# Kernel optimization log

Hardware: AMD Instinct MI355X
Metric: run time of the kernel (lower is better)

Reference implementation:

```python
import jax, jax.numpy as jnp
import numpy as np

EMBED = 1024
HEADS = 16
HEAD_DIM = EMBED // HEADS


def setup_inputs() -> dict:
    key = jax.random.key(0)
    ks = jax.random.split(key, 7)
    B, S = 4, 2048
    q = jax.random.normal(ks[0], (B, S, EMBED), dtype=jnp.float32)
    k = jax.random.normal(ks[1], (B, S, EMBED), dtype=jnp.float32)
    v = jax.random.normal(ks[2], (B, S, EMBED), dtype=jnp.float32)
    # causal mask, broadcast over heads: [B, 1, S, S]
    mask = jnp.broadcast_to(jnp.tril(jnp.ones((S, S), dtype=jnp.int32))[None, None], (B, 1, S, S))
    scale = 1.0 / np.sqrt(EMBED)
    w_q = jax.random.normal(ks[3], (EMBED, EMBED), dtype=jnp.float32) * scale
    w_k = jax.random.normal(ks[4], (EMBED, EMBED), dtype=jnp.float32) * scale
    w_v = jax.random.normal(ks[5], (EMBED, EMBED), dtype=jnp.float32) * scale
    w_o = jax.random.normal(ks[6], (EMBED, EMBED), dtype=jnp.float32) * scale
    return {"q": q, "k": k, "v": v, "mask": mask,
            "w_q": w_q, "w_k": w_k, "w_v": w_v, "w_o": w_o}


def reference(q, k, v, mask, w_q, w_k, w_v, w_o):
    B, S, _ = q.shape
    # Linear projections (torch Linear: x @ W^T), split into heads: [B,H,S,D]
    def proj(x, w):
        return (x @ w.T).reshape(B, -1, HEADS, HEAD_DIM).transpose(0, 2, 1, 3)
    qh, kh, vh = proj(q, w_q), proj(k, w_k), proj(v, w_v)
    scores = jnp.einsum('bhqd,bhkd->bhqk', qh, kh) / jnp.sqrt(jnp.float32(HEAD_DIM))
    scores = jnp.where(mask == 0, jnp.float32(-1e9), scores)
    attn = jax.nn.softmax(scores, axis=-1)
    # dropout is identity in eval/reference mode
    x = jnp.einsum('bhqk,bhkd->bhqd', attn, vh)  # [B,H,S,D]
    x = x.transpose(0, 2, 1, 3).reshape(B, S, HEADS * HEAD_DIM)
    return x @ w_o.T
```

## Files before the change

kernel.cpp:

```cpp
#include <hip/hip_runtime.h>

typedef unsigned short u16;
typedef __attribute__((ext_vector_type(8))) short v8s;
typedef __attribute__((ext_vector_type(4))) float v4f;

#define S_LEN  2048
#define NHEADS 16
#define DHEAD  64
#define EMB    1024

#if __has_builtin(__builtin_amdgcn_exp2f)
#define EXP2F __builtin_amdgcn_exp2f
#else
#define EXP2F exp2f
#endif

__device__ __forceinline__ u16 f32_bf16(float f) {
  union { float f; unsigned u; } x; x.f = f;
  unsigned r = x.u + 0x7fffu + ((x.u >> 16) & 1u);
  return (u16)(r >> 16);
}

__device__ __forceinline__ void async16(const void* g, void* l) {
  __builtin_amdgcn_global_load_lds(
      (const __attribute__((address_space(1))) unsigned int*)g,
      (__attribute__((address_space(3))) unsigned int*)l, 16, 0, 0);
}

__global__ __launch_bounds__(256) void cvt_all(
    const float4* __restrict__ s0, const float4* __restrict__ s1,
    const float4* __restrict__ s2, const float4* __restrict__ s3,
    const float4* __restrict__ s4, const float4* __restrict__ s5,
    const float4* __restrict__ s6,
    u16* __restrict__ d0, u16* __restrict__ d1,
    u16* __restrict__ d2, u16* __restrict__ d3,
    u16* __restrict__ d4, u16* __restrict__ d5,
    u16* __restrict__ d6, int nbig, int nsmall) {
  const int y = blockIdx.y;
  const float4* s; u16* d;
  switch (y) {
    case 0: s = s0; d = d0; break;  case 1: s = s1; d = d1; break;
    case 2: s = s2; d = d2; break;  case 3: s = s3; d = d3; break;
    case 4: s = s4; d = d4; break;  case 5: s = s5; d = d5; break;
    default: s = s6; d = d6; break;
  }
  const int n8 = (y < 3) ? nbig : nsmall;
  for (int i = blockIdx.x * 256 + threadIdx.x; i < n8; i += gridDim.x * 256) {
    const float4 lo = s[2 * i];
    const float4 hi = s[2 * i + 1];
    v8s o;
    o[0] = (short)f32_bf16(lo.x); o[1] = (short)f32_bf16(lo.y);
    o[2] = (short)f32_bf16(lo.z); o[3] = (short)f32_bf16(lo.w);
    o[4] = (short)f32_bf16(hi.x); o[5] = (short)f32_bf16(hi.y);
    o[6] = (short)f32_bf16(hi.z); o[7] = (short)f32_bf16(hi.w);
    *(v8s*)(d + (size_t)i * 8) = o;
  }
}

template <int MODE>
__global__ __launch_bounds__(1024, 4) void gemm2ph(
    const u16* __restrict__ A, const u16* __restrict__ W0,
    const u16* __restrict__ W1, const u16* __restrict__ W2,
    u16* __restrict__ Cq, u16* __restrict__ Ck, u16* __restrict__ Cv,
    float* __restrict__ Cf, int mtiles) {
  const int K = 1024;
  const int NKT = 16;
  __shared__ __align__(16) u16 lA[2][256 * 64];
  __shared__ __align__(16) u16 lB[2][128 * 64];
  const int t = threadIdx.x;
  const int lane = t & 63, wv = t >> 6;
  const int wm = wv >> 2, wn = wv & 3;
  const int qr = lane >> 4, cl = lane & 15;

  const int nwg = gridDim.x;
  const int sid = (blockIdx.x & 7) * (nwg >> 3) + (blockIdx.x >> 3);
  const int bm = sid % mtiles, bn = sid / mtiles;
  const int m0 = bm << 8, n0 = bn << 7;
  const int sec = (MODE == 0) ? (m0 >> 13) : 0;
  const u16* W =
      (MODE == 0) ? ((sec == 0) ? W0 : (sec == 1) ? W1 : W2) : W0;

  v4f acc[4][2];
#pragma unroll
  for (int i = 0; i < 4; ++i)
#pragma unroll
    for (int j = 0; j < 2; ++j) acc[i][j] = (v4f){0.f, 0.f, 0.f, 0.f};

  const int srow = t >> 3;
  const int swe = ((t & 7) ^ (srow & 7)) << 3;
  const u16* aS0 = A + (size_t)(m0 + srow) * K + swe;
  const u16* aS1 = A + (size_t)(m0 + 128 + srow) * K + swe;
  const u16* bS  = W + (size_t)(n0 + srow) * K + swe;

  async16(aS0, &lA[0][t << 3]);
  async16(aS1, &lA[0][(t + 1024) << 3]);
  async16(bS,  &lB[0][t << 3]);
  __syncthreads();

  for (int kt = 0; kt < NKT; ++kt) {
    const int cur = kt & 1;
    if (kt + 1 < NKT) {
      const int off = (kt + 1) << 6;
      async16(aS0 + off, &lA[1 - cur][t << 3]);
      async16(aS1 + off, &lA[1 - cur][(t + 1024) << 3]);
      async16(bS + off,  &lB[1 - cur][t << 3]);
    }
    v8s a[4][2], b[2][2];
#pragma unroll
    for (int mf = 0; mf < 4; ++mf)
#pragma unroll
      for (int kh = 0; kh < 2; ++kh) {
        const int R = wm * 64 + mf * 16 + cl;
        a[mf][kh] =
            *(const v8s*)&lA[cur][R * 64 + ((((kh << 2) + qr) ^ (R & 7)) << 3)];
      }
#pragma unroll
    for (int nf = 0; nf < 2; ++nf)
#pragma unroll
      for (int kh = 0; kh < 2; ++kh) {
        const int R = wn * 32 + nf * 16 + cl;
        b[nf][kh] =
            *(const v8s*)&lB[cur][R * 64 + ((((kh << 2) + qr) ^ (R & 7)) << 3)];
      }
    __builtin_amdgcn_s_setprio(1);
#pragma unroll
    for (int kh = 0; kh < 2; ++kh)
#pragma unroll
      for (int mf = 0; mf < 4; ++mf)
#pragma unroll
        for (int nf = 0; nf < 2; ++nf)
          acc[mf][nf] = __builtin_amdgcn_mfma_f32_16x16x32_bf16(
              a[mf][kh], b[nf][kh], acc[mf][nf], 0, 0, 0);
    __builtin_amdgcn_s_setprio(0);
    __syncthreads();
  }

  if constexpr (MODE == 0) {
    u16* C = (sec == 0) ? Cq : (sec == 1) ? Ck : Cv;
#pragma unroll
    for (int mf = 0; mf < 4; ++mf)
#pragma unroll
      for (int nf = 0; nf < 2; ++nf)
#pragma unroll
        for (int r = 0; r < 4; ++r) {
          const int mloc = (m0 & 8191) + wm * 64 + mf * 16 + qr * 4 + r;
          const int n = n0 + wn * 32 + nf * 16 + cl;
          const int bb = mloc >> 11, s = mloc & (S_LEN - 1);
          const int h = n >> 6, d = n & (DHEAD - 1);
          const size_t idx =
              (sec < 2) ? (((size_t)bb * NHEADS + h) * S_LEN + s) * DHEAD + d
                        : (((size_t)bb * NHEADS + h) * DHEAD + d) * S_LEN + s;
          C[idx] = f32_bf16(acc[mf][nf][r]);
        }
  } else {
#pragma unroll
    for (int mf = 0; mf < 4; ++mf)
#pragma unroll
      for (int nf = 0; nf < 2; ++nf)
#pragma unroll
        for (int r = 0; r < 4; ++r) {
          const int m = m0 + wm * 64 + mf * 16 + qr * 4 + r;
          const int n = n0 + wn * 32 + nf * 16 + cl;
          Cf[(size_t)m * 1024 + n] = acc[mf][nf][r];
        }
  }
}

__global__ __launch_bounds__(256, 2) void attn_causal(
    const u16* __restrict__ Qp, const u16* __restrict__ Kp,
    const u16* __restrict__ VpT, u16* __restrict__ Out) {
  __shared__ __align__(16) u16 lK[2][2][64 * 64];
  __shared__ __align__(16) u16 lV[2][2][64 * 64];
  __shared__ __align__(16) u16 pb[4][32 * 64];
  const int t = threadIdx.x;
  const int lane = t & 63, w = t >> 6;
  const int qr = lane >> 4, cl = lane & 15;
  const int id = blockIdx.x;
  const int col = (id & 7) + ((id >> 6) << 3);
  const int pair = (id >> 3) & 7;
  const int h = col & 15, b = col >> 4;
  const size_t bh = ((size_t)b * NHEADS + h) * S_LEN * DHEAD;
  const u16* Qb = Qp + bh;
  const u16* Kb = Kp + bh;
  const u16* Vb = VpT + bh;

  v8s vone;
#pragma unroll
  for (int j = 0; j < 8; ++j) vone[j] = (short)0x3F80;
  const float SC = 0.125f * 1.4426950408889634f;

#define STAGE_T(TILE, GP, SL)                                                 \
  do {                                                                        \
    const int kn_ = (TILE) << 6;                                              \
    _Pragma("unroll") for (int i_ = 0; i_ < 2; ++i_) {                        \
      const int c_ = t + (i_ << 8);                                           \
      const int krow_ = c_ >> 3, kdc_ = (c_ & 7) ^ (krow_ & 7);               \
      async16(Kb + (size_t)(kn_ + krow_) * DHEAD + kdc_ * 8,                  \
              &lK[GP][SL][(w * 64 + (i_ << 8)) * 8]);                         \
      const int vd_ = c_ >> 3, vkc_ = (c_ & 7) ^ (vd_ & 7);                   \
      async16(Vb + (size_t)vd_ * S_LEN + kn_ + vkc_ * 8,                      \
              &lV[GP][SL][(w * 64 + (i_ << 8)) * 8]);                         \
    }                                                                         \
  } while (0)

  for (int phase = 0; phase < 2; ++phase) {
    const int qt = phase == 0 ? (15 - pair) : pair;
    const int q0 = qt << 7;
    const int wr0 = q0 + w * 32;

    v8s aq[2][2];
#pragma unroll
    for (int mf = 0; mf < 2; ++mf)
#pragma unroll
      for (int kf = 0; kf < 2; ++kf)
        aq[mf][kf] = *(const v8s*)(Qb + (size_t)(wr0 + mf * 16 + cl) * DHEAD +
                                   kf * 32 + qr * 8);

    v4f o[2][4], lac[2];
#pragma unroll
    for (int mf = 0; mf < 2; ++mf) {
      lac[mf] = (v4f){0.f, 0.f, 0.f, 0.f};
#pragma unroll
      for (int nf = 0; nf < 4; ++nf) o[mf][nf] = (v4f){0.f, 0.f, 0.f, 0.f};
    }

    const int ngrp = qt + 1;
    __syncthreads();
    STAGE_T(0, 0, 0);
    STAGE_T(1, 0, 1);

    for (int g = 0; g < ngrp; ++g) {
      const int gp = g & 1;
      __syncthreads();
      if (g + 1 < ngrp) {
        STAGE_T(2 * g + 2, 1 - gp, 0);
        STAGE_T(2 * g + 3, 1 - gp, 1);
      }
#pragma unroll
      for (int sl = 0; sl < 2; ++sl) {
        const int kt = 2 * g + sl;
        const int k0 = kt << 6;
        if (k0 > wr0 + 31) continue;
        const u16* lKc = &lK[gp][sl][0];
        const u16* lVc = &lV[gp][sl][0];

        v4f sacc[2][4];
#pragma unroll
        for (int mf = 0; mf < 2; ++mf)
#pragma unroll
          for (int ni = 0; ni < 4; ++ni) sacc[mf][ni] = (v4f){0.f, 0.f, 0.f, 0.f};
#pragma unroll
        for (int kf = 0; kf < 2; ++kf)
#pragma unroll
          for (int ni = 0; ni < 4; ++ni) {
            const v8s bk = *(const v8s*)&lKc[((ni * 16 + cl) * 8 +
                                             (((kf << 2) + qr) ^ (cl & 7))) * 8];
            sacc[0][ni] = __builtin_amdgcn_mfma_f32_16x16x32_bf16(
                aq[0][kf], bk, sacc[0][ni], 0, 0, 0);
            sacc[1][ni] = __builtin_amdgcn_mfma_f32_16x16x32_bf16(
                aq[1][kf], bk, sacc[1][ni], 0, 0, 0);
          }

#pragma unroll
        for (int mf = 0; mf < 2; ++mf) {
          const int rowb0 = wr0 + mf * 16;
          if (k0 + 63 <= rowb0) {
#pragma unroll
            for (int ni = 0; ni < 4; ++ni) {
              const int kc = ni * 2 + (cl >> 3);
#pragma unroll
              for (int r = 0; r < 4; ++r) {
                const float e = EXP2F(sacc[mf][ni][r] * SC);
                pb[w][((kc * 32 + mf * 16 + r * 4 + qr) << 3) + (cl & 7)] =
                    (u16)(__float_as_uint(e) >> 16);
              }
            }
          } else {
            const int rowb = rowb0 + qr * 4;
#pragma unroll
            for (int ni = 0; ni < 4; ++ni) {
              const int colk = k0 + ni * 16 + cl;
              const int kc = ni * 2 + (cl >> 3);
#pragma unroll
              for (int r = 0; r < 4; ++r) {
                float e = EXP2F(sacc[mf][ni][r] * SC);
                if (colk > rowb + r) e = 0.f;
                pb[w][((kc * 32 + mf * 16 + r * 4 + qr) << 3) + (cl & 7)] =
                    (u16)(__float_as_uint(e) >> 16);
              }
            }
          }
        }

#pragma unroll
        for (int kf = 0; kf < 2; ++kf) {
          const int kc = (kf << 2) + qr;
          const int sig0 = ((cl & 3) << 2) + (cl >> 2);
          const v8s ap0 = *(const v8s*)&pb[w][((kc * 32 + sig0) << 3)];
          const v8s ap1 = *(const v8s*)&pb[w][((kc * 32 + 16 + sig0) << 3)];
          lac[0] = __builtin_amdgcn_mfma_f32_16x16x32_bf16(ap0, vone, lac[0], 0, 0, 0);
          lac[1] = __builtin_amdgcn_mfma_f32_16x16x32_bf16(ap1, vone, lac[1], 0, 0, 0);
#pragma unroll
          for (int nf = 0; nf < 4; ++nf) {
            const v8s bv = *(const v8s*)&lVc[((nf * 16 + cl) * 8 +
                                             (kc ^ (cl & 7))) * 8];
            o[0][nf] = __builtin_amdgcn_mfma_f32_16x16x32_bf16(ap0, bv, o[0][nf], 0, 0, 0);
            o[1][nf] = __builtin_amdgcn_mfma_f32_16x16x32_bf16(ap1, bv, o[1][nf], 0, 0, 0);
          }
        }
      }
    }

#pragma unroll
    for (int mf = 0; mf < 2; ++mf) {
      float inv[4];
#pragma unroll
      for (int r = 0; r < 4; ++r) inv[r] = 1.0f / lac[mf][r];
#pragma unroll
      for (int nf = 0; nf < 4; ++nf)
#pragma unroll
        for (int r = 0; r < 4; ++r) {
          const int row = wr0 + mf * 16 + qr * 4 + r;
          const int colo = h * DHEAD + nf * 16 + cl;
          Out[((size_t)b * S_LEN + row) * EMB + colo] = f32_bf16(o[mf][nf][r] * inv[r]);
        }
    }
  }
#undef STAGE_T
}

extern "C" void kernel_launch(void* const* d_in, const int* in_sizes, int n_in,
                              void* d_out, int out_size, void* d_ws, size_t ws_size,
                              hipStream_t stream) {
  (void)in_sizes; (void)n_in; (void)out_size; (void)ws_size;
  const float* q  = (const float*)d_in[0];
  const float* k  = (const float*)d_in[1];
  const float* v  = (const float*)d_in[2];
  const float* wq = (const float*)d_in[4];
  const float* wk = (const float*)d_in[5];
  const float* wv = (const float*)d_in[6];
  const float* wo = (const float*)d_in[7];
  float* out = (float*)d_out;

  const size_t MT = (size_t)4 * S_LEN * EMB;
  const size_t WT = (size_t)EMB * EMB;
  u16* p = (u16*)d_ws;
  u16* xq = p; p += MT;
  u16* xk = p; p += MT;
  u16* xv = p; p += MT;
  u16* wqb = p; p += WT;
  u16* wkb = p; p += WT;
  u16* wvb = p; p += WT;
  u16* wob = p; p += WT;
  u16* Qp = p; p += MT;
  u16* Kp = p; p += MT;
  u16* Vp = p; p += MT;
  u16* Ao = xq;

  hipLaunchKernelGGL(cvt_all, dim3(512, 7), dim3(256), 0, stream,
                     (const float4*)q, (const float4*)k, (const float4*)v,
                     (const float4*)wq, (const float4*)wk, (const float4*)wv,
                     (const float4*)wo,
                     xq, xk, xv, wqb, wkb, wvb, wob,
                     (int)(MT / 8), (int)(WT / 8));
  hipLaunchKernelGGL((gemm2ph<0>), dim3(768), dim3(1024), 0, stream,
                     xq, wqb, wkb, wvb, Qp, Kp, Vp, (float*)nullptr, 96);
  hipLaunchKernelGGL(attn_causal, dim3(512), dim3(256), 0, stream,
                     Qp, Kp, Vp, Ao);
  hipLaunchKernelGGL((gemm2ph<1>), dim3(256), dim3(1024), 0, stream,
                     Ao, wob, (const u16*)nullptr, (const u16*)nullptr,
                     (u16*)nullptr, (u16*)nullptr, (u16*)nullptr, out, 32);
}
```

Measured before the change: 352.3 us.

## Shrink GEMM tiles to 128x128 and use 8 waves of 16 rows in attention

The projection GEMMs move from 256x128 tiles with 1024 threads to 128x128 tiles with 512 threads, doubling the grid and halving LDS per block. The attention kernel goes from 4 waves of 32 query rows each to 8 waves of 16 rows each, so per-wave accumulators and P buffers shrink and one K/V staging load per thread covers the tile. The goal is more parallelism and better occupancy, at the cost of less data reuse per K/V tile load and more global traffic in the GEMMs.

```diff
diff --git a/kernel.cpp b/kernel.cpp
--- a/kernel.cpp
+++ b/kernel.cpp
@@ -58,14 +58,14 @@
 }
 
 template <int MODE>
-__global__ __launch_bounds__(1024, 4) void gemm2ph(
+__global__ __launch_bounds__(512, 2) void gemm2ph(
     const u16* __restrict__ A, const u16* __restrict__ W0,
     const u16* __restrict__ W1, const u16* __restrict__ W2,
     u16* __restrict__ Cq, u16* __restrict__ Ck, u16* __restrict__ Cv,
     float* __restrict__ Cf, int mtiles) {
   const int K = 1024;
   const int NKT = 16;
-  __shared__ __align__(16) u16 lA[2][256 * 64];
+  __shared__ __align__(16) u16 lA[2][128 * 64];
   __shared__ __align__(16) u16 lB[2][128 * 64];
   const int t = threadIdx.x;
   const int lane = t & 63, wv = t >> 6;
@@ -75,7 +75,7 @@
   const int nwg = gridDim.x;
   const int sid = (blockIdx.x & 7) * (nwg >> 3) + (blockIdx.x >> 3);
   const int bm = sid % mtiles, bn = sid / mtiles;
-  const int m0 = bm << 8, n0 = bn << 7;
+  const int m0 = bm << 7, n0 = bn << 7;
   const int sec = (MODE == 0) ? (m0 >> 13) : 0;
   const u16* W =
       (MODE == 0) ? ((sec == 0) ? W0 : (sec == 1) ? W1 : W2) : W0;
@@ -87,23 +87,31 @@
     for (int j = 0; j < 2; ++j) acc[i][j] = (v4f){0.f, 0.f, 0.f, 0.f};
 
   const int srow = t >> 3;
-  const int swe = ((t & 7) ^ (srow & 7)) << 3;
-  const u16* aS0 = A + (size_t)(m0 + srow) * K + swe;
-  const u16* aS1 = A + (size_t)(m0 + 128 + srow) * K + swe;
-  const u16* bS  = W + (size_t)(n0 + srow) * K + swe;
-
-  async16(aS0, &lA[0][t << 3]);
-  async16(aS1, &lA[0][(t + 1024) << 3]);
-  async16(bS,  &lB[0][t << 3]);
+  const int sw = ((t & 7) ^ (srow & 7)) << 3;
+  const u16* aS[2];
+  const u16* bS[2];
+#pragma unroll
+  for (int u = 0; u < 2; ++u) {
+    aS[u] = A + (size_t)(m0 + srow + u * 64) * K + sw;
+    bS[u] = W + (size_t)(n0 + srow + u * 64) * K + sw;
+  }
+
+#pragma unroll
+  for (int u = 0; u < 2; ++u) async16(aS[u], &lA[0][(t + (u << 9)) << 3]);
+#pragma unroll
+  for (int u = 0; u < 2; ++u) async16(bS[u], &lB[0][(t + (u << 9)) << 3]);
   __syncthreads();
 
   for (int kt = 0; kt < NKT; ++kt) {
     const int cur = kt & 1;
     if (kt + 1 < NKT) {
       const int off = (kt + 1) << 6;
-      async16(aS0 + off, &lA[1 - cur][t << 3]);
-      async16(aS1 + off, &lA[1 - cur][(t + 1024) << 3]);
-      async16(bS + off,  &lB[1 - cur][t << 3]);
+#pragma unroll
+      for (int u = 0; u < 2; ++u)
+        async16(aS[u] + off, &lA[1 - cur][(t + (u << 9)) << 3]);
+#pragma unroll
+      for (int u = 0; u < 2; ++u)
+        async16(bS[u] + off, &lB[1 - cur][(t + (u << 9)) << 3]);
     }
     v8s a[4][2], b[2][2];
 #pragma unroll
@@ -166,12 +174,12 @@
   }
 }
 
-__global__ __launch_bounds__(256, 2) void attn_causal(
+__global__ __launch_bounds__(512, 2) void attn_causal(
     const u16* __restrict__ Qp, const u16* __restrict__ Kp,
     const u16* __restrict__ VpT, u16* __restrict__ Out) {
   __shared__ __align__(16) u16 lK[2][2][64 * 64];
   __shared__ __align__(16) u16 lV[2][2][64 * 64];
-  __shared__ __align__(16) u16 pb[4][32 * 64];
+  __shared__ __align__(16) u16 pb[8][16 * 64];
   const int t = threadIdx.x;
   const int lane = t & 63, w = t >> 6;
   const int qr = lane >> 4, cl = lane & 15;
@@ -192,37 +200,25 @@
 #define STAGE_T(TILE, GP, SL)                                                 \
   do {                                                                        \
     const int kn_ = (TILE) << 6;                                              \
-    _Pragma("unroll") for (int i_ = 0; i_ < 2; ++i_) {                        \
-      const int c_ = t + (i_ << 8);                                           \
-      const int krow_ = c_ >> 3, kdc_ = (c_ & 7) ^ (krow_ & 7);               \
-      async16(Kb + (size_t)(kn_ + krow_) * DHEAD + kdc_ * 8,                  \
-              &lK[GP][SL][(w * 64 + (i_ << 8)) * 8]);                         \
-      const int vd_ = c_ >> 3, vkc_ = (c_ & 7) ^ (vd_ & 7);                   \
-      async16(Vb + (size_t)vd_ * S_LEN + kn_ + vkc_ * 8,                      \
-              &lV[GP][SL][(w * 64 + (i_ << 8)) * 8]);                         \
-    }                                                                         \
+    const int r_ = t >> 3, c_ = (t & 7) ^ (r_ & 7);                           \
+    async16(Kb + (size_t)(kn_ + r_) * DHEAD + c_ * 8, &lK[GP][SL][t * 8]);    \
+    async16(Vb + (size_t)r_ * S_LEN + kn_ + c_ * 8, &lV[GP][SL][t * 8]);      \
   } while (0)
 
   for (int phase = 0; phase < 2; ++phase) {
     const int qt = phase == 0 ? (15 - pair) : pair;
     const int q0 = qt << 7;
-    const int wr0 = q0 + w * 32;
-
-    v8s aq[2][2];
-#pragma unroll
-    for (int mf = 0; mf < 2; ++mf)
-#pragma unroll
-      for (int kf = 0; kf < 2; ++kf)
-        aq[mf][kf] = *(const v8s*)(Qb + (size_t)(wr0 + mf * 16 + cl) * DHEAD +
-                                   kf * 32 + qr * 8);
-
-    v4f o[2][4], lac[2];
-#pragma unroll
-    for (int mf = 0; mf < 2; ++mf) {
-      lac[mf] = (v4f){0.f, 0.f, 0.f, 0.f};
-#pragma unroll
-      for (int nf = 0; nf < 4; ++nf) o[mf][nf] = (v4f){0.f, 0.f, 0.f, 0.f};
-    }
+    const int wr0 = q0 + w * 16;
+
+    v8s aq[2];
+#pragma unroll
+    for (int kf = 0; kf < 2; ++kf)
+      aq[kf] = *(const v8s*)(Qb + (size_t)(wr0 + cl) * DHEAD + kf * 32 + qr * 8);
+
+    v4f o[4], lac;
+    lac = (v4f){0.f, 0.f, 0.f, 0.f};
+#pragma unroll
+    for (int nf = 0; nf < 4; ++nf) o[nf] = (v4f){0.f, 0.f, 0.f, 0.f};
 
     const int ngrp = qt + 1;
     __syncthreads();
@@ -240,54 +236,46 @@
       for (int sl = 0; sl < 2; ++sl) {
         const int kt = 2 * g + sl;
         const int k0 = kt << 6;
-        if (k0 > wr0 + 31) continue;
+        if (k0 > wr0 + 15) continue;
         const u16* lKc = &lK[gp][sl][0];
         const u16* lVc = &lV[gp][sl][0];
 
-        v4f sacc[2][4];
-#pragma unroll
-        for (int mf = 0; mf < 2; ++mf)
-#pragma unroll
-          for (int ni = 0; ni < 4; ++ni) sacc[mf][ni] = (v4f){0.f, 0.f, 0.f, 0.f};
+        v4f sacc[4];
+#pragma unroll
+        for (int ni = 0; ni < 4; ++ni) sacc[ni] = (v4f){0.f, 0.f, 0.f, 0.f};
 #pragma unroll
         for (int kf = 0; kf < 2; ++kf)
 #pragma unroll
           for (int ni = 0; ni < 4; ++ni) {
             const v8s bk = *(const v8s*)&lKc[((ni * 16 + cl) * 8 +
                                              (((kf << 2) + qr) ^ (cl & 7))) * 8];
-            sacc[0][ni] = __builtin_amdgcn_mfma_f32_16x16x32_bf16(
-                aq[0][kf], bk, sacc[0][ni], 0, 0, 0);
-            sacc[1][ni] = __builtin_amdgcn_mfma_f32_16x16x32_bf16(
-                aq[1][kf], bk, sacc[1][ni], 0, 0, 0);
+            sacc[ni] = __builtin_amdgcn_mfma_f32_16x16x32_bf16(
+                aq[kf], bk, sacc[ni], 0, 0, 0);
           }
 
-#pragma unroll
-        for (int mf = 0; mf < 2; ++mf) {
-          const int rowb0 = wr0 + mf * 16;
-          if (k0 + 63 <= rowb0) {
-#pragma unroll
-            for (int ni = 0; ni < 4; ++ni) {
-              const int kc = ni * 2 + (cl >> 3);
-#pragma unroll
-              for (int r = 0; r < 4; ++r) {
-                const float e = EXP2F(sacc[mf][ni][r] * SC);
-                pb[w][((kc * 32 + mf * 16 + r * 4 + qr) << 3) + (cl & 7)] =
-                    (u16)(__float_as_uint(e) >> 16);
-              }
+        if (k0 + 63 <= wr0) {
+#pragma unroll
+          for (int ni = 0; ni < 4; ++ni) {
+            const int kc = ni * 2 + (cl >> 3);
+#pragma unroll
+            for (int r = 0; r < 4; ++r) {
+              const float e = EXP2F(sacc[ni][r] * SC);
+              pb[w][((kc * 16 + r * 4 + qr) << 3) + (cl & 7)] =
+                  (u16)(__float_as_uint(e) >> 16);
             }
-          } else {
-            const int rowb = rowb0 + qr * 4;
-#pragma unroll
-            for (int ni = 0; ni < 4; ++ni) {
-              const int colk = k0 + ni * 16 + cl;
-              const int kc = ni * 2 + (cl >> 3);
-#pragma unroll
-              for (int r = 0; r < 4; ++r) {
-                float e = EXP2F(sacc[mf][ni][r] * SC);
-                if (colk > rowb + r) e = 0.f;
-                pb[w][((kc * 32 + mf * 16 + r * 4 + qr) << 3) + (cl & 7)] =
-                    (u16)(__float_as_uint(e) >> 16);
-              }
+          }
+        } else {
+          const int rowb = wr0 + qr * 4;
+#pragma unroll
+          for (int ni = 0; ni < 4; ++ni) {
+            const int colk = k0 + ni * 16 + cl;
+            const int kc = ni * 2 + (cl >> 3);
+#pragma unroll
+            for (int r = 0; r < 4; ++r) {
+              float e = EXP2F(sacc[ni][r] * SC);
+              if (colk > rowb + r) e = 0.f;
+              pb[w][((kc * 16 + r * 4 + qr) << 3) + (cl & 7)] =
+                  (u16)(__float_as_uint(e) >> 16);
             }
           }
         }
@@ -296,35 +284,29 @@
         for (int kf = 0; kf < 2; ++kf) {
           const int kc = (kf << 2) + qr;
           const int sig0 = ((cl & 3) << 2) + (cl >> 2);
-          const v8s ap0 = *(const v8s*)&pb[w][((kc * 32 + sig0) << 3)];
-          const v8s ap1 = *(const v8s*)&pb[w][((kc * 32 + 16 + sig0) << 3)];
-          lac[0] = __builtin_amdgcn_mfma_f32_16x16x32_bf16(ap0, vone, lac[0], 0, 0, 0);
-          lac[1] = __builtin_amdgcn_mfma_f32_16x16x32_bf16(ap1, vone, lac[1], 0, 0, 0);
+          const v8s ap = *(const v8s*)&pb[w][((kc * 16 + sig0) << 3)];
+          lac = __builtin_amdgcn_mfma_f32_16x16x32_bf16(ap, vone, lac, 0, 0, 0);
 #pragma unroll
           for (int nf = 0; nf < 4; ++nf) {
             const v8s bv = *(const v8s*)&lVc[((nf * 16 + cl) * 8 +
                                              (kc ^ (cl & 7))) * 8];
-            o[0][nf] = __builtin_amdgcn_mfma_f32_16x16x32_bf16(ap0, bv, o[0][nf], 0, 0, 0);
-            o[1][nf] = __builtin_amdgcn_mfma_f32_16x16x32_bf16(ap1, bv, o[1][nf], 0, 0, 0);
+            o[nf] = __builtin_amdgcn_mfma_f32_16x16x32_bf16(ap, bv, o[nf], 0, 0, 0);
           }
         }
       }
     }
 
-#pragma unroll
-    for (int mf = 0; mf < 2; ++mf) {
-      float inv[4];
-#pragma unroll
-      for (int r = 0; r < 4; ++r) inv[r] = 1.0f / lac[mf][r];
-#pragma unroll
-      for (int nf = 0; nf < 4; ++nf)
-#pragma unroll
-        for (int r = 0; r < 4; ++r) {
-          const int row = wr0 + mf * 16 + qr * 4 + r;
-          const int colo = h * DHEAD + nf * 16 + cl;
-          Out[((size_t)b * S_LEN + row) * EMB + colo] = f32_bf16(o[mf][nf][r] * inv[r]);
-        }
-    }
+    float inv[4];
+#pragma unroll
+    for (int r = 0; r < 4; ++r) inv[r] = 1.0f / lac[r];
+#pragma unroll
+    for (int nf = 0; nf < 4; ++nf)
+#pragma unroll
+      for (int r = 0; r < 4; ++r) {
+        const int row = wr0 + qr * 4 + r;
+        const int colo = h * DHEAD + nf * 16 + cl;
+        Out[((size_t)b * S_LEN + row) * EMB + colo] = f32_bf16(o[nf][r] * inv[r]);
+      }
   }
 #undef STAGE_T
 }
@@ -363,11 +345,11 @@
                      (const float4*)wo,
                      xq, xk, xv, wqb, wkb, wvb, wob,
                      (int)(MT / 8), (int)(WT / 8));
-  hipLaunchKernelGGL((gemm2ph<0>), dim3(768), dim3(1024), 0, stream,
-                     xq, wqb, wkb, wvb, Qp, Kp, Vp, (float*)nullptr, 96);
-  hipLaunchKernelGGL(attn_causal, dim3(512), dim3(256), 0, stream,
+  hipLaunchKernelGGL((gemm2ph<0>), dim3(1536), dim3(512), 0, stream,
+                     xq, wqb, wkb, wvb, Qp, Kp, Vp, (float*)nullptr, 192);
+  hipLaunchKernelGGL(attn_causal, dim3(512), dim3(512), 0, stream,
                      Qp, Kp, Vp, Ao);
-  hipLaunchKernelGGL((gemm2ph<1>), dim3(256), dim3(1024), 0, stream,
+  hipLaunchKernelGGL((gemm2ph<1>), dim3(512), dim3(512), 0, stream,
                      Ao, wob, (const u16*)nullptr, (const u16*)nullptr,
-                     (u16*)nullptr, (u16*)nullptr, (u16*)nullptr, out, 32);
-}
+                     (u16*)nullptr, (u16*)nullptr, (u16*)nullptr, out, 64);
+}
```

Result: no change. 345.7 us (-1.9%).

## Restructure GEMMs to 128x128 tiles with intra-block split-K over 8 waves

Applied to the files above, without the earlier changes.

Replaces the 1024-thread 256x128-tile GEMM with a 512-thread 128x128-tile kernel. The eight waves are split into two K-halves of each 64-wide K step, and each wave computes a 64x64 sub-tile. The two halves' partial accumulators are then reduced through LDS before the epilogue. This doubles the number of workgroups and gives each wave a larger per-wave output tile, aiming for better register reuse and occupancy. The cost is an extra LDS reduction pass and half of the waves going idle during the epilogue.

```diff
diff --git a/kernel.cpp b/kernel.cpp
--- a/kernel.cpp
+++ b/kernel.cpp
@@ -58,93 +58,120 @@
 }
 
 template <int MODE>
-__global__ __launch_bounds__(1024, 4) void gemm2ph(
+__global__ __launch_bounds__(512, 2) void gemmks(
     const u16* __restrict__ A, const u16* __restrict__ W0,
     const u16* __restrict__ W1, const u16* __restrict__ W2,
     u16* __restrict__ Cq, u16* __restrict__ Ck, u16* __restrict__ Cv,
     float* __restrict__ Cf, int mtiles) {
   const int K = 1024;
   const int NKT = 16;
-  __shared__ __align__(16) u16 lA[2][256 * 64];
-  __shared__ __align__(16) u16 lB[2][128 * 64];
+  __shared__ __align__(16) u16 ldsbuf[32768];
+  u16* const lA0 = ldsbuf;
+  u16* const lB0 = ldsbuf + 16384;
   const int t = threadIdx.x;
   const int lane = t & 63, wv = t >> 6;
-  const int wm = wv >> 2, wn = wv & 3;
+  const int kh = wv >> 2;
+  const int sp = wv & 3;
+  const int wm = sp >> 1, wn = sp & 1;
   const int qr = lane >> 4, cl = lane & 15;
 
   const int nwg = gridDim.x;
   const int sid = (blockIdx.x & 7) * (nwg >> 3) + (blockIdx.x >> 3);
   const int bm = sid % mtiles, bn = sid / mtiles;
-  const int m0 = bm << 8, n0 = bn << 7;
+  const int m0 = bm << 7, n0 = bn << 7;
   const int sec = (MODE == 0) ? (m0 >> 13) : 0;
   const u16* W =
       (MODE == 0) ? ((sec == 0) ? W0 : (sec == 1) ? W1 : W2) : W0;
 
-  v4f acc[4][2];
+  v4f acc[4][4];
 #pragma unroll
   for (int i = 0; i < 4; ++i)
 #pragma unroll
-    for (int j = 0; j < 2; ++j) acc[i][j] = (v4f){0.f, 0.f, 0.f, 0.f};
+    for (int j = 0; j < 4; ++j) acc[i][j] = (v4f){0.f, 0.f, 0.f, 0.f};
 
   const int srow = t >> 3;
-  const int swe = ((t & 7) ^ (srow & 7)) << 3;
-  const u16* aS0 = A + (size_t)(m0 + srow) * K + swe;
-  const u16* aS1 = A + (size_t)(m0 + 128 + srow) * K + swe;
-  const u16* bS  = W + (size_t)(n0 + srow) * K + swe;
-
-  async16(aS0, &lA[0][t << 3]);
-  async16(aS1, &lA[0][(t + 1024) << 3]);
-  async16(bS,  &lB[0][t << 3]);
+  const int sw = ((t & 7) ^ (srow & 7)) << 3;
+  const u16* aS[2];
+  const u16* bS[2];
+#pragma unroll
+  for (int u = 0; u < 2; ++u) {
+    aS[u] = A + (size_t)(m0 + srow + u * 64) * K + sw;
+    bS[u] = W + (size_t)(n0 + srow + u * 64) * K + sw;
+  }
+
+  int aOff[4], bOff[4];
+#pragma unroll
+  for (int f = 0; f < 4; ++f) {
+    const int Ra = wm * 64 + f * 16 + cl;
+    aOff[f] = Ra * 64 + ((((kh << 2) + qr) ^ (Ra & 7)) << 3);
+    const int Rb = wn * 64 + f * 16 + cl;
+    bOff[f] = Rb * 64 + ((((kh << 2) + qr) ^ (Rb & 7)) << 3);
+  }
+
+#pragma unroll
+  for (int u = 0; u < 2; ++u) async16(aS[u], lA0 + ((t + (u << 9)) << 3));
+#pragma unroll
+  for (int u = 0; u < 2; ++u) async16(bS[u], lB0 + ((t + (u << 9)) << 3));
   __syncthreads();
 
   for (int kt = 0; kt < NKT; ++kt) {
     const int cur = kt & 1;
     if (kt + 1 < NKT) {
       const int off = (kt + 1) << 6;
-      async16(aS0 + off, &lA[1 - cur][t << 3]);
-      async16(aS1 + off, &lA[1 - cur][(t + 1024) << 3]);
-      async16(bS + off,  &lB[1 - cur][t << 3]);
+      u16* dA = lA0 + (1 - cur) * 8192;
+      u16* dB = lB0 + (1 - cur) * 8192;
+#pragma unroll
+      for (int u = 0; u < 2; ++u) async16(aS[u] + off, dA + ((t + (u << 9)) << 3));
+#pragma unroll
+      for (int u = 0; u < 2; ++u) async16(bS[u] + off, dB + ((t + (u << 9)) << 3));
     }
-    v8s a[4][2], b[2][2];
+    const u16* rA = lA0 + cur * 8192;
+    const u16* rB = lB0 + cur * 8192;
+    v8s a[4], b[4];
+#pragma unroll
+    for (int f = 0; f < 4; ++f) a[f] = *(const v8s*)(rA + aOff[f]);
+#pragma unroll
+    for (int f = 0; f < 4; ++f) b[f] = *(const v8s*)(rB + bOff[f]);
+    __builtin_amdgcn_s_setprio(1);
 #pragma unroll
     for (int mf = 0; mf < 4; ++mf)
 #pragma unroll
-      for (int kh = 0; kh < 2; ++kh) {
-        const int R = wm * 64 + mf * 16 + cl;
-        a[mf][kh] =
-            *(const v8s*)&lA[cur][R * 64 + ((((kh << 2) + qr) ^ (R & 7)) << 3)];
-      }
-#pragma unroll
-    for (int nf = 0; nf < 2; ++nf)
-#pragma unroll
-      for (int kh = 0; kh < 2; ++kh) {
-        const int R = wn * 32 + nf * 16 + cl;
-        b[nf][kh] =
-            *(const v8s*)&lB[cur][R * 64 + ((((kh << 2) + qr) ^ (R & 7)) << 3)];
-      }
-    __builtin_amdgcn_s_setprio(1);
-#pragma unroll
-    for (int kh = 0; kh < 2; ++kh)
-#pragma unroll
-      for (int mf = 0; mf < 4; ++mf)
-#pragma unroll
-        for (int nf = 0; nf < 2; ++nf)
-          acc[mf][nf] = __builtin_amdgcn_mfma_f32_16x16x32_bf16(
-              a[mf][kh], b[nf][kh], acc[mf][nf], 0, 0, 0);
+      for (int nf = 0; nf < 4; ++nf)
+        acc[mf][nf] = __builtin_amdgcn_mfma_f32_16x16x32_bf16(
+            a[mf], b[nf], acc[mf][nf], 0, 0, 0);
     __builtin_amdgcn_s_setprio(0);
     __syncthreads();
   }
 
+  v4f* red = (v4f*)ldsbuf;
+  if (kh == 1) {
+#pragma unroll
+    for (int mf = 0; mf < 4; ++mf)
+#pragma unroll
+      for (int nf = 0; nf < 4; ++nf)
+        red[sp * 1024 + (mf * 4 + nf) * 64 + qr * 16 + cl] = acc[mf][nf];
+  }
+  __syncthreads();
+  if (kh == 1) return;
+#pragma unroll
+  for (int mf = 0; mf < 4; ++mf)
+#pragma unroll
+    for (int nf = 0; nf < 4; ++nf) {
+      const v4f r2 = red[sp * 1024 + (mf * 4 + nf) * 64 + qr * 16 + cl];
+#pragma unroll
+      for (int r = 0; r < 4; ++r) acc[mf][nf][r] += r2[r];
+    }
+
   if constexpr (MODE == 0) {
     u16* C = (sec == 0) ? Cq : (sec == 1) ? Ck : Cv;
 #pragma unroll
     for (int mf = 0; mf < 4; ++mf)
 #pragma unroll
-      for (int nf = 0; nf < 2; ++nf)
+      for (int nf = 0; nf < 4; ++nf)
 #pragma unroll
         for (int r = 0; r < 4; ++r) {
           const int mloc = (m0 & 8191) + wm * 64 + mf * 16 + qr * 4 + r;
-          const int n = n0 + wn * 32 + nf * 16 + cl;
+          const int n = n0 + wn * 64 + nf * 16 + cl;
           const int bb = mloc >> 11, s = mloc & (S_LEN - 1);
           const int h = n >> 6, d = n & (DHEAD - 1);
           const size_t idx =
@@ -156,11 +183,11 @@
 #pragma unroll
     for (int mf = 0; mf < 4; ++mf)
 #pragma unroll
-      for (int nf = 0; nf < 2; ++nf)
+      for (int nf = 0; nf < 4; ++nf)
 #pragma unroll
         for (int r = 0; r < 4; ++r) {
           const int m = m0 + wm * 64 + mf * 16 + qr * 4 + r;
-          const int n = n0 + wn * 32 + nf * 16 + cl;
+          const int n = n0 + wn * 64 + nf * 16 + cl;
           Cf[(size_t)m * 1024 + n] = acc[mf][nf][r];
         }
   }
@@ -363,11 +390,11 @@
                      (const float4*)wo,
                      xq, xk, xv, wqb, wkb, wvb, wob,
                      (int)(MT / 8), (int)(WT / 8));
-  hipLaunchKernelGGL((gemm2ph<0>), dim3(768), dim3(1024), 0, stream,
-                     xq, wqb, wkb, wvb, Qp, Kp, Vp, (float*)nullptr, 96);
+  hipLaunchKernelGGL((gemmks<0>), dim3(1536), dim3(512), 0, stream,
+                     xq, wqb, wkb, wvb, Qp, Kp, Vp, (float*)nullptr, 192);
   hipLaunchKernelGGL(attn_causal, dim3(512), dim3(256), 0, stream,
                      Qp, Kp, Vp, Ao);
-  hipLaunchKernelGGL((gemm2ph<1>), dim3(256), dim3(1024), 0, stream,
+  hipLaunchKernelGGL((gemmks<1>), dim3(512), dim3(512), 0, stream,
                      Ao, wob, (const u16*)nullptr, (const u16*)nullptr,
-                     (u16*)nullptr, (u16*)nullptr, (u16*)nullptr, out, 32);
-}
+                     (u16*)nullptr, (u16*)nullptr, (u16*)nullptr, out, 64);
+}
```

Result: no change. 348.7 us (-1.0%).
